# Performance work log

Measured on AMD Instinct MI355X. Metric: run time of the kernel, lower is better.

## Reference

```python
import jax, jax.numpy as jnp
import numpy as np

N = 16384
N_IN = 64
N_H = 64
DIMS = [N_IN, N_H + 200, N_H + 100, N_H]  # 64 -> 264 -> 164 -> 64 (args.l == 2 path)


def setup_inputs() -> dict:
    key = jax.random.key(0)
    ks = jax.random.split(key, 16)
    inp = {
        "seq1": jax.random.normal(ks[0], (1, N, N_IN), dtype=jnp.float32),
        "seq2": jax.random.normal(ks[1], (1, N, N_IN), dtype=jnp.float32),
        # dense adjacency, scaled ~1/n like a row-normalized GCN adjacency
        "adj": jax.random.uniform(ks[2], (1, N, N), dtype=jnp.float32) / N,
        "samp_bias1": jnp.zeros((1, N), dtype=jnp.float32),
        "samp_bias2": jnp.zeros((1, N), dtype=jnp.float32),
    }
    # GCN layer params: Linear(in, out, bias=False) weight + per-layer bias
    for i in range(3):
        din, dout = DIMS[i], DIMS[i + 1]
        inp[f"w{i+1}"] = jax.random.normal(ks[3 + 2 * i], (din, dout), dtype=jnp.float32) * (1.0 / np.sqrt(din))
        inp[f"b{i+1}"] = jnp.zeros((dout,), dtype=jnp.float32)
    # Discriminator bilinear f_k = nn.Bilinear(n_h, n_h, 1): weight [n_h, n_h], bias scalar
    inp["wd"] = jax.random.normal(ks[10], (N_H, N_H), dtype=jnp.float32) * (1.0 / np.sqrt(N_H))
    inp["bd"] = jnp.zeros((), dtype=jnp.float32)
    return inp


def _encoder(seq, adj, ws, bs):
    h = seq  # [1, n, d]
    for w, b in zip(ws, bs):
        # GCN layer: act(adj @ (X W) + b)
        h = jax.nn.relu(jnp.einsum('bnm,bmd->bnd', adj, jnp.einsum('bnk,kd->bnd', h, w)) + b)
    return h


def reference(seq1, seq2, adj, samp_bias1, samp_bias2, w1, b1, w2, b2, w3, b3, wd, bd):
    ws, bs = (w1, w2, w3), (b1, b2, b3)
    h_1 = _encoder(seq1, adj, ws, bs)                 # [1, n, n_h]
    c = jax.nn.sigmoid(jnp.mean(h_1, axis=1))         # AvgReadout + sigmoid -> [1, n_h]
    h_2 = _encoder(seq2, adj, ws, bs)                 # [1, n, n_h]
    # Bilinear discriminator: sc[b, i] = h[b, i, :] @ Wd @ c[b, :] + bd (+ samp_bias)
    cw = jnp.einsum('bd,ed->be', c, wd)               # Wd acts on (h, c) pair -> [1, n_h]
    sc_1 = jnp.einsum('bnd,bd->bn', h_1, cw) + bd + samp_bias1
    sc_2 = jnp.einsum('bnd,bd->bn', h_2, cw) + bd + samp_bias2
    return jnp.concatenate([sc_1, sc_2], axis=1)      # [1, 2n]
```

## Files before the change

### kernel.cpp

```cpp
#include <hip/hip_runtime.h>
#include <hip/hip_bf16.h>

#define NN 16384

using f32x4  = __attribute__((ext_vector_type(4))) float;
using bf16x8 = __attribute__((ext_vector_type(8))) __bf16;
using u16x8  = __attribute__((ext_vector_type(8))) unsigned short;

__device__ __forceinline__ void split2(float x, unsigned short& h, unsigned short& l) {
  unsigned u  = __float_as_uint(x);
  unsigned hu = u & 0xFFFF0000u;
  float lf = x - __uint_as_float(hu);
  __bf16 lb = (__bf16)lf;
  h = (unsigned short)(hu >> 16);
  l = __builtin_bit_cast(unsigned short, lb);
}

__device__ __forceinline__ void gload_lds16(const void* g, void* l) {
  __builtin_amdgcn_global_load_lds(
      (const __attribute__((address_space(1))) unsigned*)g,
      (__attribute__((address_space(3))) unsigned*)l, 16, 0, 0);
}

__global__ void prep_seq(const float* __restrict__ seq1, const float* __restrict__ seq2,
                         unsigned short* __restrict__ Shi, unsigned short* __restrict__ Slo) {
  const int tid = threadIdx.x;
  const int r0  = blockIdx.x * 64;
  const float* seq = blockIdx.y ? seq2 : seq1;
  __shared__ float t[64][65];
  #pragma unroll
  for (int i = 0; i < 16; ++i) {
    int row = i * 4 + (tid >> 6);
    t[row][tid & 63] = seq[(long)(r0 + row) * 64 + (tid & 63)];
  }
  __syncthreads();
  #pragma unroll
  for (int i = 0; i < 16; ++i) {
    int col = i * 4 + (tid >> 6);
    int rr  = tid & 63;
    unsigned short h, l;
    split2(t[rr][col], h, l);
    long o = (long)(blockIdx.y * 64 + col) * NN + r0 + rr;
    Shi[o] = h; Slo[o] = l;
  }
}

__launch_bounds__(256, 2)
__global__ void gemm_adj(const float* __restrict__ A,
                         const unsigned short* __restrict__ Bhi,
                         const unsigned short* __restrict__ Blo,
                         float* __restrict__ P, int ccols, int klen) {
  __shared__ unsigned short Ahs[128 * 40], Als[128 * 40], Xhs[128 * 40], Xls[128 * 40];
  const int tid  = threadIdx.x;
  const int lane = tid & 63;
  const int wave = tid >> 6;
  const int wr = wave & 1;
  const int wc = wave >> 1;
  const int rtile = blockIdx.x * 128;
  const int ctile = blockIdx.y * 128;
  const int kbase = blockIdx.z * klen;

  const int srow  = tid >> 1;
  const int shalf = tid & 1;
  const int wbase = srow * 40 + shalf * 16;

  const float* aptr = A + (long)(rtile + srow) * NN + kbase + shalf * 16;
  const unsigned short* bhp = Bhi + (long)(ctile + srow) * NN + kbase + shalf * 16;
  const unsigned short* blp = Blo + (long)(ctile + srow) * NN + kbase + shalf * 16;

  f32x4 acc[4][4] = {};

  f32x4 a0 = *(const f32x4*)(aptr + 0);
  f32x4 a1 = *(const f32x4*)(aptr + 4);
  f32x4 a2 = *(const f32x4*)(aptr + 8);
  f32x4 a3 = *(const f32x4*)(aptr + 12);
  uint4 bh0 = *(const uint4*)(bhp);
  uint4 bh1 = *(const uint4*)(bhp + 8);
  uint4 bl0 = *(const uint4*)(blp);
  uint4 bl1 = *(const uint4*)(blp + 8);
  aptr += 32; bhp += 32; blp += 32;

  const int nsteps = klen / 32;
  for (int ks = 0; ks < nsteps; ++ks) {
    u16x8 h0, h1, l0, l1;
    #pragma unroll
    for (int i = 0; i < 16; ++i) {
      float x = i < 4 ? a0[i] : (i < 8 ? a1[i - 4] : (i < 12 ? a2[i - 8] : a3[i - 12]));
      unsigned short hh, ll;
      split2(x, hh, ll);
      if (i < 8) { h0[i] = hh; l0[i] = ll; }
      else       { h1[i - 8] = hh; l1[i - 8] = ll; }
    }
    __syncthreads();
    *(u16x8*)&Ahs[wbase + 0] = h0;
    *(u16x8*)&Ahs[wbase + 8] = h1;
    *(u16x8*)&Als[wbase + 0] = l0;
    *(u16x8*)&Als[wbase + 8] = l1;
    *(uint4*)&Xhs[wbase + 0] = bh0;
    *(uint4*)&Xhs[wbase + 8] = bh1;
    *(uint4*)&Xls[wbase + 0] = bl0;
    *(uint4*)&Xls[wbase + 8] = bl1;
    if (ks + 1 < nsteps) {
      a0 = *(const f32x4*)(aptr + 0);
      a1 = *(const f32x4*)(aptr + 4);
      a2 = *(const f32x4*)(aptr + 8);
      a3 = *(const f32x4*)(aptr + 12);
      bh0 = *(const uint4*)(bhp);
      bh1 = *(const uint4*)(bhp + 8);
      bl0 = *(const uint4*)(blp);
      bl1 = *(const uint4*)(blp + 8);
      aptr += 32; bhp += 32; blp += 32;
    }
    __syncthreads();
    bf16x8 ahf[4], alf[4];
    #pragma unroll
    for (int ni = 0; ni < 4; ++ni) {
      int ar  = wr * 64 + ni * 16 + (lane & 15);
      int off = ar * 40 + (lane >> 4) * 8;
      ahf[ni] = *(const bf16x8*)&Ahs[off];
      alf[ni] = *(const bf16x8*)&Als[off];
    }
    #pragma unroll
    for (int mi = 0; mi < 4; ++mi) {
      int xc  = wc * 64 + mi * 16 + (lane & 15);
      int off = xc * 40 + (lane >> 4) * 8;
      bf16x8 xh = *(const bf16x8*)&Xhs[off];
      bf16x8 xl = *(const bf16x8*)&Xls[off];
      #pragma unroll
      for (int ni = 0; ni < 4; ++ni) {
        acc[mi][ni] = __builtin_amdgcn_mfma_f32_16x16x32_bf16(xh, ahf[ni], acc[mi][ni], 0, 0, 0);
        acc[mi][ni] = __builtin_amdgcn_mfma_f32_16x16x32_bf16(xl, ahf[ni], acc[mi][ni], 0, 0, 0);
        acc[mi][ni] = __builtin_amdgcn_mfma_f32_16x16x32_bf16(xh, alf[ni], acc[mi][ni], 0, 0, 0);
      }
    }
  }
  float* out = P + (long)blockIdx.z * ccols * NN;
  #pragma unroll
  for (int mi = 0; mi < 4; ++mi) {
    int xc = ctile + wc * 64 + mi * 16 + ((lane >> 4) << 2);
    #pragma unroll
    for (int ni = 0; ni < 4; ++ni) {
      int ar = rtile + wr * 64 + ni * 16 + (lane & 15);
      #pragma unroll
      for (int j = 0; j < 4; ++j)
        out[(long)(xc + j) * NN + ar] = acc[mi][ni][j];
    }
  }
}

__launch_bounds__(256, 3)
__global__ void gemm_v(const float* __restrict__ A,
                       const unsigned short* __restrict__ Xg,
                       const float* __restrict__ cs,
                       float* __restrict__ P, int ccols, int klen, int nY) {
  __shared__ unsigned short As[128 * 64];
  __shared__ unsigned short Xs[2][128 * 64];
  const int tid  = threadIdx.x;
  const int lane = tid & 63;
  const int wave = tid >> 6;
  const int wr = wave & 1;
  const int wc = wave >> 1;

  int bid = blockIdx.x;
  int lin = (bid & 7) * ((int)gridDim.x >> 3) + (bid >> 3);
  const int by = lin % nY;
  const int bx = (lin / nY) & 127;
  const int bz = lin / (nY * 128);
  const int rtile = bx * 128;
  const int ctile = by * 128;
  const int kbase = bz * klen;

  const int arow0  = wave * 32 + (lane >> 3);
  const int ac     = lane & 7;
  const int awslot = ac ^ (lane >> 3);
  const float* aptr = A + (long)(rtile + arow0) * NN + kbase + ac * 8;

  const int xrow0 = wave * 32 + (lane >> 3);
  const int cx    = (lane & 7) ^ (lane >> 3);
  const unsigned short* xptr = Xg + (long)(ctile + xrow0) * NN + kbase + cx * 8;

  f32x4 acc[4][4] = {};
  f32x4 areg[4][2];

  #pragma unroll
  for (int t = 0; t < 4; ++t) {
    const float* ap = aptr + (long)t * 8 * NN;
    areg[t][0] = *(const f32x4*)ap;
    areg[t][1] = *(const f32x4*)(ap + 4);
    gload_lds16(xptr + (long)t * 8 * NN, &Xs[0][(wave * 4 + t) * 512]);
  }
  aptr += 64; xptr += 64;
  __syncthreads();

  int cur = 0;
  const int nsteps = klen / 64;
  for (int ks = 0; ks < nsteps; ++ks) {
    u16x8 wv[4];
    #pragma unroll
    for (int t = 0; t < 4; ++t) {
      #pragma unroll
      for (int i = 0; i < 8; ++i) {
        float a = (i < 4) ? areg[t][0][i] : areg[t][1][i - 4];
        float v = fmaf(a, 16384.f, -0.5f);
        wv[t][i] = __builtin_bit_cast(unsigned short, (__bf16)v);
      }
    }
    __syncthreads();
    #pragma unroll
    for (int t = 0; t < 4; ++t)
      *(u16x8*)&As[(arow0 + t * 8) * 64 + awslot * 8] = wv[t];
    if (ks + 1 < nsteps) {
      #pragma unroll
      for (int t = 0; t < 4; ++t) {
        gload_lds16(xptr + (long)t * 8 * NN, &Xs[cur ^ 1][(wave * 4 + t) * 512]);
        const float* ap = aptr + (long)t * 8 * NN;
        areg[t][0] = *(const f32x4*)ap;
        areg[t][1] = *(const f32x4*)(ap + 4);
      }
      aptr += 64; xptr += 64;
    }
    __syncthreads();
    #pragma unroll
    for (int mk = 0; mk < 2; ++mk) {
      bf16x8 af[4];
      #pragma unroll
      for (int ni = 0; ni < 4; ++ni) {
        int ar = wr * 64 + ni * 16 + (lane & 15);
        int slot = (mk * 4 + (lane >> 4)) ^ (ar & 7);
        af[ni] = *(const bf16x8*)&As[ar * 64 + slot * 8];
      }
      #pragma unroll
      for (int mi = 0; mi < 4; ++mi) {
        int xr = wc * 64 + mi * 16 + (lane & 15);
        int slot = (mk * 4 + (lane >> 4)) ^ (xr & 7);
        bf16x8 xf = *(const bf16x8*)&Xs[cur][xr * 64 + slot * 8];
        #pragma unroll
        for (int ni = 0; ni < 4; ++ni)
          acc[mi][ni] = __builtin_amdgcn_mfma_f32_16x16x32_bf16(xf, af[ni], acc[mi][ni], 0, 0, 0);
      }
    }
    cur ^= 1;
  }

  const float scl = 1.f / 16384.f;
  float* out = P + (long)bz * ccols * NN;
  #pragma unroll
  for (int mi = 0; mi < 4; ++mi) {
    int xc = ctile + wc * 64 + mi * 16 + ((lane >> 4) << 2);
    float dc[4];
    #pragma unroll
    for (int j = 0; j < 4; ++j) dc[j] = (bz == 0) ? 0.5f * cs[xc + j] : 0.f;
    #pragma unroll
    for (int ni = 0; ni < 4; ++ni) {
      int ar = rtile + wr * 64 + ni * 16 + (lane & 15);
      #pragma unroll
      for (int j = 0; j < 4; ++j)
        out[(long)(xc + j) * NN + ar] = (acc[mi][ni][j] + dc[j]) * scl;
    }
  }
}

__global__ void post1a(const float* __restrict__ P, const float* __restrict__ w1,
                       const float* __restrict__ b1, float* __restrict__ H1T) {
  const int r = blockIdx.x * 256 + threadIdx.x;
  const int e = blockIdx.y;
  for (int c = 0; c < 4; ++c) {
    const int j0 = c * 66;
    float acc[66];
    #pragma unroll
    for (int jj = 0; jj < 66; ++jj) acc[jj] = b1[j0 + jj];
    for (int k = 0; k < 64; ++k) {
      float tv = 0.f;
      #pragma unroll
      for (int z = 0; z < 4; ++z)
        tv += P[(long)(z * 128 + e * 64 + k) * NN + r];
      #pragma unroll
      for (int jj = 0; jj < 66; ++jj)
        acc[jj] = fmaf(tv, w1[k * 264 + j0 + jj], acc[jj]);
    }
    #pragma unroll
    for (int jj = 0; jj < 66; ++jj)
      H1T[(long)(e * 264 + j0 + jj) * NN + r] = fmaxf(acc[jj], 0.f);
  }
}

__global__ void post1b(const float* __restrict__ H1T, const float* __restrict__ w2,
                       unsigned short* __restrict__ G) {
  const int r  = blockIdx.x * 256 + threadIdx.x;
  const int e  = blockIdx.y;
  const int q0 = blockIdx.z * 41;
  float acc[41] = {};
  for (int j = 0; j < 264; ++j) {
    float h = H1T[(long)(e * 264 + j) * NN + r];
    #pragma unroll
    for (int qq = 0; qq < 41; ++qq)
      acc[qq] = fmaf(h, w2[j * 164 + q0 + qq], acc[qq]);
  }
  #pragma unroll
  for (int qq = 0; qq < 41; ++qq)
    G[(long)(e * 192 + q0 + qq) * NN + r] =
        __builtin_bit_cast(unsigned short, (__bf16)acc[qq]);
  if (blockIdx.z == 3) {
    for (int q = 164; q < 192; ++q)
      G[(long)(e * 192 + q) * NN + r] = 0;
  }
}

__global__ void colsum_bf16(const unsigned short* __restrict__ X, float* __restrict__ cs) {
  const int c = blockIdx.x;
  const unsigned short* row = X + (long)c * NN;
  float s = 0.f;
  for (int i = threadIdx.x; i < NN; i += 256)
    s += __uint_as_float((unsigned)row[i] << 16);
  __shared__ float red[256];
  red[threadIdx.x] = s;
  __syncthreads();
  for (int off = 128; off > 0; off >>= 1) {
    if (threadIdx.x < off) red[threadIdx.x] += red[threadIdx.x + off];
    __syncthreads();
  }
  if (threadIdx.x == 0) cs[c] = red[0];
}

__global__ void post2(const float* __restrict__ P, const float* __restrict__ w3,
                      const float* __restrict__ b2, unsigned short* __restrict__ F) {
  const int r = blockIdx.x * 256 + threadIdx.x;
  const int e = blockIdx.y;
  float f[64] = {};
  for (int j = 0; j < 164; ++j) {
    float h = P[(long)(e * 192 + j) * NN + r] + P[(long)(384 + e * 192 + j) * NN + r] + b2[j];
    h = fmaxf(h, 0.f);
    #pragma unroll
    for (int q = 0; q < 64; ++q) f[q] = fmaf(h, w3[j * 64 + q], f[q]);
  }
  #pragma unroll
  for (int q = 0; q < 64; ++q)
    F[(long)(e * 64 + q) * NN + r] = __builtin_bit_cast(unsigned short, (__bf16)f[q]);
}

__global__ void post3(const float* __restrict__ P, const float* __restrict__ b3,
                      float* __restrict__ H3T) {
  const int r = blockIdx.x * 256 + threadIdx.x;
  const int e = blockIdx.y;
  #pragma unroll
  for (int q = 0; q < 64; ++q) {
    float v = b3[q];
    #pragma unroll
    for (int z = 0; z < 4; ++z)
      v += P[(long)(z * 128 + e * 64 + q) * NN + r];
    H3T[(long)(e * 64 + q) * NN + r] = fmaxf(v, 0.f);
  }
}

__global__ void colsum(const float* __restrict__ H3T, float* __restrict__ sums) {
  const int c = blockIdx.x;
  const float* row = H3T + (long)c * NN;
  float s = 0.f;
  for (int i = threadIdx.x; i < NN; i += 256) s += row[i];
  __shared__ float red[256];
  red[threadIdx.x] = s;
  __syncthreads();
  for (int off = 128; off > 0; off >>= 1) {
    if (threadIdx.x < off) red[threadIdx.x] += red[threadIdx.x + off];
    __syncthreads();
  }
  if (threadIdx.x == 0) sums[c] = red[0];
}

__global__ void make_cw(const float* __restrict__ sums, const float* __restrict__ wd,
                        float* __restrict__ cw) {
  __shared__ float cv[64];
  const int t = threadIdx.x;
  cv[t] = 1.f / (1.f + expf(-sums[t] / 16384.f));
  __syncthreads();
  float a = 0.f;
  for (int d = 0; d < 64; ++d) a += cv[d] * wd[t * 64 + d];
  cw[t] = a;
}

__global__ void score(const float* __restrict__ H3T, const float* __restrict__ cw,
                      const float* __restrict__ bdp, const float* __restrict__ sb1,
                      const float* __restrict__ sb2, float* __restrict__ out) {
  const int idx = blockIdx.x * 256 + threadIdx.x;
  const int e = idx >> 14, r = idx & (NN - 1);
  float acc = bdp[0] + (e ? sb2[r] : sb1[r]);
  const float* base = H3T + (long)e * 64 * NN + r;
  #pragma unroll
  for (int j = 0; j < 64; ++j) acc = fmaf(base[(long)j * NN], cw[j], acc);
  out[idx] = acc;
}

extern "C" void kernel_launch(void* const* d_in, const int* in_sizes, int n_in,
                              void* d_out, int out_size, void* d_ws, size_t ws_size,
                              hipStream_t stream) {
  const float* seq1 = (const float*)d_in[0];
  const float* seq2 = (const float*)d_in[1];
  const float* adj  = (const float*)d_in[2];
  const float* sb1  = (const float*)d_in[3];
  const float* sb2  = (const float*)d_in[4];
  const float* w1   = (const float*)d_in[5];
  const float* b1   = (const float*)d_in[6];
  const float* w2   = (const float*)d_in[7];
  const float* b2   = (const float*)d_in[8];
  const float* w3   = (const float*)d_in[9];
  const float* b3   = (const float*)d_in[10];
  const float* wd   = (const float*)d_in[11];
  const float* bd   = (const float*)d_in[12];
  float* out = (float*)d_out;

  char* ws = (char*)d_ws;
  unsigned short* Shi = (unsigned short*)(ws + 0);
  unsigned short* Slo = (unsigned short*)(ws + 4194304);
  float*          Pp  = (float*)(ws + 8388608);
  unsigned short* G   = (unsigned short*)(ws + 58720256);
  float*          H1T = (float*)(ws + 71303168);
  unsigned short* F   = (unsigned short*)(ws + 105906176);
  float*          H3T = (float*)(ws + 110100480);
  float*          csG = (float*)(ws + 118489088);
  float*          csF = (float*)(ws + 118490624);
  float*          sums= (float*)(ws + 118491136);
  float*          cw  = (float*)(ws + 118491392);

  prep_seq   <<<dim3(256, 2), 256, 0, stream>>>(seq1, seq2, Shi, Slo);
  gemm_adj   <<<dim3(128, 1, 4), 256, 0, stream>>>(adj, Shi, Slo, Pp, 128, 4096);
  post1a     <<<dim3(64, 2), 256, 0, stream>>>(Pp, w1, b1, H1T);
  post1b     <<<dim3(64, 2, 4), 256, 0, stream>>>(H1T, w2, G);
  colsum_bf16<<<384, 256, 0, stream>>>(G, csG);
  gemm_v     <<<768, 256, 0, stream>>>(adj, G, csG, Pp, 384, 8192, 3);
  post2      <<<dim3(64, 2), 256, 0, stream>>>(Pp, w3, b2, F);
  colsum_bf16<<<128, 256, 0, stream>>>(F, csF);
  gemm_v     <<<512, 256, 0, stream>>>(adj, F, csF, Pp, 128, 4096, 1);
  post3      <<<dim3(64, 2), 256, 0, stream>>>(Pp, b3, H3T);
  colsum     <<<64, 256, 0, stream>>>(H3T, sums);
  make_cw    <<<1, 64, 0, stream>>>(sums, wd, cw);
  score      <<<128, 256, 0, stream>>>(H3T, cw, bd, sb1, sb2, out);
}
```

Before: 1.250 ms.

## Quantize adjacency to bf16 once in first GEMM and reuse across layers

```diff
diff --git a/kernel.cpp b/kernel.cpp
--- a/kernel.cpp
+++ b/kernel.cpp
@@ -6,15 +6,6 @@
 using f32x4  = __attribute__((ext_vector_type(4))) float;
 using bf16x8 = __attribute__((ext_vector_type(8))) __bf16;
 using u16x8  = __attribute__((ext_vector_type(8))) unsigned short;
-
-__device__ __forceinline__ void split2(float x, unsigned short& h, unsigned short& l) {
-  unsigned u  = __float_as_uint(x);
-  unsigned hu = u & 0xFFFF0000u;
-  float lf = x - __uint_as_float(hu);
-  __bf16 lb = (__bf16)lf;
-  h = (unsigned short)(hu >> 16);
-  l = __builtin_bit_cast(unsigned short, lb);
-}
 
 __device__ __forceinline__ void gload_lds16(const void* g, void* l) {
   __builtin_amdgcn_global_load_lds(
@@ -22,8 +13,42 @@
       (__attribute__((address_space(3))) unsigned*)l, 16, 0, 0);
 }
 
+__device__ __forceinline__ unsigned short bf16r(float x) {
+  return __builtin_bit_cast(unsigned short, (__bf16)x);
+}
+
+__global__ void zero_cs(float* __restrict__ csS) {
+  if (threadIdx.x < 128) csS[threadIdx.x] = 0.f;
+}
+
+__global__ void seqsum(const float* __restrict__ seq1, const float* __restrict__ seq2,
+                       float* __restrict__ csS) {
+  const int e = blockIdx.x >> 4, chunk = blockIdx.x & 15;
+  const float* seq = e ? seq2 : seq1;
+  const int g = threadIdx.x >> 4;
+  const int q = threadIdx.x & 15;
+  f32x4 acc = {};
+  for (int i = 0; i < 64; ++i) {
+    int r = chunk * 1024 + i * 16 + g;
+    acc += *(const f32x4*)(seq + (long)r * 64 + q * 4);
+  }
+  __shared__ f32x4 red[256];
+  red[threadIdx.x] = acc;
+  __syncthreads();
+  if (threadIdx.x < 64) {
+    int d = threadIdx.x;
+    float s = 0.f;
+    #pragma unroll
+    for (int g2 = 0; g2 < 16; ++g2) {
+      f32x4 v = red[g2 * 16 + (d >> 2)];
+      s += v[d & 3];
+    }
+    atomicAdd(&csS[e * 64 + d], s);
+  }
+}
+
 __global__ void prep_seq(const float* __restrict__ seq1, const float* __restrict__ seq2,
-                         unsigned short* __restrict__ Shi, unsigned short* __restrict__ Slo) {
+                         unsigned short* __restrict__ Shi) {
   const int tid = threadIdx.x;
   const int r0  = blockIdx.x * 64;
   const float* seq = blockIdx.y ? seq2 : seq1;
@@ -38,118 +63,124 @@
   for (int i = 0; i < 16; ++i) {
     int col = i * 4 + (tid >> 6);
     int rr  = tid & 63;
-    unsigned short h, l;
-    split2(t[rr][col], h, l);
-    long o = (long)(blockIdx.y * 64 + col) * NN + r0 + rr;
-    Shi[o] = h; Slo[o] = l;
-  }
-}
-
-__launch_bounds__(256, 2)
-__global__ void gemm_adj(const float* __restrict__ A,
-                         const unsigned short* __restrict__ Bhi,
-                         const unsigned short* __restrict__ Blo,
-                         float* __restrict__ P, int ccols, int klen) {
-  __shared__ unsigned short Ahs[128 * 40], Als[128 * 40], Xhs[128 * 40], Xls[128 * 40];
+    Shi[(long)(blockIdx.y * 64 + col) * NN + r0 + rr] = bf16r(t[rr][col]);
+  }
+}
+
+__launch_bounds__(256, 3)
+__global__ void gemm1(const float* __restrict__ A,
+                      const unsigned short* __restrict__ Xg,
+                      const float* __restrict__ cs,
+                      float* __restrict__ P,
+                      unsigned short* __restrict__ Vg) {
+  __shared__ unsigned short As[128 * 64];
+  __shared__ unsigned short Xs[2][128 * 64];
   const int tid  = threadIdx.x;
   const int lane = tid & 63;
   const int wave = tid >> 6;
   const int wr = wave & 1;
   const int wc = wave >> 1;
-  const int rtile = blockIdx.x * 128;
-  const int ctile = blockIdx.y * 128;
-  const int kbase = blockIdx.z * klen;
-
-  const int srow  = tid >> 1;
-  const int shalf = tid & 1;
-  const int wbase = srow * 40 + shalf * 16;
-
-  const float* aptr = A + (long)(rtile + srow) * NN + kbase + shalf * 16;
-  const unsigned short* bhp = Bhi + (long)(ctile + srow) * NN + kbase + shalf * 16;
-  const unsigned short* blp = Blo + (long)(ctile + srow) * NN + kbase + shalf * 16;
+
+  int bid = blockIdx.x;
+  int lin = (bid & 7) * ((int)gridDim.x >> 3) + (bid >> 3);
+  const int bx = lin & 127;
+  const int bz = lin >> 7;
+  const int rtile = bx * 128;
+  const int kbase = bz * 4096;
+
+  const int arow0  = wave * 32 + (lane >> 3);
+  const int ac     = lane & 7;
+  const int awslot = ac ^ (lane >> 3);
+  const float* aptr = A + (long)(rtile + arow0) * NN + kbase + ac * 8;
+  unsigned short* vptr = Vg + (long)(rtile + arow0) * NN + kbase + ac * 8;
+
+  const int cx = (lane & 7) ^ (lane >> 3);
+  const unsigned short* xptr = Xg + (long)arow0 * NN + kbase + cx * 8;
 
   f32x4 acc[4][4] = {};
-
-  f32x4 a0 = *(const f32x4*)(aptr + 0);
-  f32x4 a1 = *(const f32x4*)(aptr + 4);
-  f32x4 a2 = *(const f32x4*)(aptr + 8);
-  f32x4 a3 = *(const f32x4*)(aptr + 12);
-  uint4 bh0 = *(const uint4*)(bhp);
-  uint4 bh1 = *(const uint4*)(bhp + 8);
-  uint4 bl0 = *(const uint4*)(blp);
-  uint4 bl1 = *(const uint4*)(blp + 8);
-  aptr += 32; bhp += 32; blp += 32;
-
-  const int nsteps = klen / 32;
+  f32x4 areg[4][2];
+
+  #pragma unroll
+  for (int t = 0; t < 4; ++t) {
+    const float* ap = aptr + (long)t * 8 * NN;
+    areg[t][0] = *(const f32x4*)ap;
+    areg[t][1] = *(const f32x4*)(ap + 4);
+    gload_lds16(xptr + (long)t * 8 * NN, &Xs[0][(wave * 4 + t) * 512]);
+  }
+  aptr += 64; xptr += 64;
+  __syncthreads();
+
+  int cur = 0;
+  const int nsteps = 4096 / 64;
   for (int ks = 0; ks < nsteps; ++ks) {
-    u16x8 h0, h1, l0, l1;
-    #pragma unroll
-    for (int i = 0; i < 16; ++i) {
-      float x = i < 4 ? a0[i] : (i < 8 ? a1[i - 4] : (i < 12 ? a2[i - 8] : a3[i - 12]));
-      unsigned short hh, ll;
-      split2(x, hh, ll);
-      if (i < 8) { h0[i] = hh; l0[i] = ll; }
-      else       { h1[i - 8] = hh; l1[i - 8] = ll; }
-    }
-    __syncthreads();
-    *(u16x8*)&Ahs[wbase + 0] = h0;
-    *(u16x8*)&Ahs[wbase + 8] = h1;
-    *(u16x8*)&Als[wbase + 0] = l0;
-    *(u16x8*)&Als[wbase + 8] = l1;
-    *(uint4*)&Xhs[wbase + 0] = bh0;
-    *(uint4*)&Xhs[wbase + 8] = bh1;
-    *(uint4*)&Xls[wbase + 0] = bl0;
-    *(uint4*)&Xls[wbase + 8] = bl1;
+    u16x8 wv[4];
+    #pragma unroll
+    for (int t = 0; t < 4; ++t) {
+      #pragma unroll
+      for (int i = 0; i < 8; ++i) {
+        float a = (i < 4) ? areg[t][0][i] : areg[t][1][i - 4];
+        wv[t][i] = bf16r(fmaf(a, 16384.f, -0.5f));
+      }
+      *(u16x8*)(vptr + (long)t * 8 * NN) = wv[t];
+    }
+    vptr += 64;
+    __syncthreads();
+    #pragma unroll
+    for (int t = 0; t < 4; ++t)
+      *(u16x8*)&As[(arow0 + t * 8) * 64 + awslot * 8] = wv[t];
     if (ks + 1 < nsteps) {
-      a0 = *(const f32x4*)(aptr + 0);
-      a1 = *(const f32x4*)(aptr + 4);
-      a2 = *(const f32x4*)(aptr + 8);
-      a3 = *(const f32x4*)(aptr + 12);
-      bh0 = *(const uint4*)(bhp);
-      bh1 = *(const uint4*)(bhp + 8);
-      bl0 = *(const uint4*)(blp);
-      bl1 = *(const uint4*)(blp + 8);
-      aptr += 32; bhp += 32; blp += 32;
-    }
-    __syncthreads();
-    bf16x8 ahf[4], alf[4];
-    #pragma unroll
-    for (int ni = 0; ni < 4; ++ni) {
-      int ar  = wr * 64 + ni * 16 + (lane & 15);
-      int off = ar * 40 + (lane >> 4) * 8;
-      ahf[ni] = *(const bf16x8*)&Ahs[off];
-      alf[ni] = *(const bf16x8*)&Als[off];
-    }
-    #pragma unroll
-    for (int mi = 0; mi < 4; ++mi) {
-      int xc  = wc * 64 + mi * 16 + (lane & 15);
-      int off = xc * 40 + (lane >> 4) * 8;
-      bf16x8 xh = *(const bf16x8*)&Xhs[off];
-      bf16x8 xl = *(const bf16x8*)&Xls[off];
+      #pragma unroll
+      for (int t = 0; t < 4; ++t) {
+        gload_lds16(xptr + (long)t * 8 * NN, &Xs[cur ^ 1][(wave * 4 + t) * 512]);
+        const float* ap = aptr + (long)t * 8 * NN;
+        areg[t][0] = *(const f32x4*)ap;
+        areg[t][1] = *(const f32x4*)(ap + 4);
+      }
+      aptr += 64; xptr += 64;
+    }
+    __syncthreads();
+    #pragma unroll
+    for (int mk = 0; mk < 2; ++mk) {
+      bf16x8 af[4];
       #pragma unroll
       for (int ni = 0; ni < 4; ++ni) {
-        acc[mi][ni] = __builtin_amdgcn_mfma_f32_16x16x32_bf16(xh, ahf[ni], acc[mi][ni], 0, 0, 0);
-        acc[mi][ni] = __builtin_amdgcn_mfma_f32_16x16x32_bf16(xl, ahf[ni], acc[mi][ni], 0, 0, 0);
-        acc[mi][ni] = __builtin_amdgcn_mfma_f32_16x16x32_bf16(xh, alf[ni], acc[mi][ni], 0, 0, 0);
-      }
-    }
-  }
-  float* out = P + (long)blockIdx.z * ccols * NN;
+        int ar = wr * 64 + ni * 16 + (lane & 15);
+        int slot = (mk * 4 + (lane >> 4)) ^ (ar & 7);
+        af[ni] = *(const bf16x8*)&As[ar * 64 + slot * 8];
+      }
+      #pragma unroll
+      for (int mi = 0; mi < 4; ++mi) {
+        int xr = wc * 64 + mi * 16 + (lane & 15);
+        int slot = (mk * 4 + (lane >> 4)) ^ (xr & 7);
+        bf16x8 xf = *(const bf16x8*)&Xs[cur][xr * 64 + slot * 8];
+        #pragma unroll
+        for (int ni = 0; ni < 4; ++ni)
+          acc[mi][ni] = __builtin_amdgcn_mfma_f32_16x16x32_bf16(xf, af[ni], acc[mi][ni], 0, 0, 0);
+      }
+    }
+    cur ^= 1;
+  }
+
+  const float scl = 1.f / 16384.f;
+  float* out = P + (long)bz * 128 * NN;
   #pragma unroll
   for (int mi = 0; mi < 4; ++mi) {
-    int xc = ctile + wc * 64 + mi * 16 + ((lane >> 4) << 2);
+    int xc = wc * 64 + mi * 16 + ((lane >> 4) << 2);
+    float dc[4];
+    #pragma unroll
+    for (int j = 0; j < 4; ++j) dc[j] = (bz == 0) ? 0.5f * cs[xc + j] : 0.f;
     #pragma unroll
     for (int ni = 0; ni < 4; ++ni) {
       int ar = rtile + wr * 64 + ni * 16 + (lane & 15);
       #pragma unroll
       for (int j = 0; j < 4; ++j)
-        out[(long)(xc + j) * NN + ar] = acc[mi][ni][j];
+        out[(long)(xc + j) * NN + ar] = (acc[mi][ni][j] + dc[j]) * scl;
     }
   }
 }
 
 __launch_bounds__(256, 3)
-__global__ void gemm_v(const float* __restrict__ A,
+__global__ void gemm23(const unsigned short* __restrict__ Va,
                        const unsigned short* __restrict__ Xg,
                        const float* __restrict__ cs,
                        float* __restrict__ P, int ccols, int klen, int nY) {
@@ -173,20 +204,17 @@
   const int arow0  = wave * 32 + (lane >> 3);
   const int ac     = lane & 7;
   const int awslot = ac ^ (lane >> 3);
-  const float* aptr = A + (long)(rtile + arow0) * NN + kbase + ac * 8;
-
-  const int xrow0 = wave * 32 + (lane >> 3);
-  const int cx    = (lane & 7) ^ (lane >> 3);
-  const unsigned short* xptr = Xg + (long)(ctile + xrow0) * NN + kbase + cx * 8;
+  const unsigned short* aptr = Va + (long)(rtile + arow0) * NN + kbase + ac * 8;
+
+  const int cx = (lane & 7) ^ (lane >> 3);
+  const unsigned short* xptr = Xg + (long)(ctile + arow0) * NN + kbase + cx * 8;
 
   f32x4 acc[4][4] = {};
-  f32x4 areg[4][2];
+  u16x8 av[4];
 
   #pragma unroll
   for (int t = 0; t < 4; ++t) {
-    const float* ap = aptr + (long)t * 8 * NN;
-    areg[t][0] = *(const f32x4*)ap;
-    areg[t][1] = *(const f32x4*)(ap + 4);
+    av[t] = *(const u16x8*)(aptr + (long)t * 8 * NN);
     gload_lds16(xptr + (long)t * 8 * NN, &Xs[0][(wave * 4 + t) * 512]);
   }
   aptr += 64; xptr += 64;
@@ -195,27 +223,15 @@
   int cur = 0;
   const int nsteps = klen / 64;
   for (int ks = 0; ks < nsteps; ++ks) {
-    u16x8 wv[4];
-    #pragma unroll
-    for (int t = 0; t < 4; ++t) {
-      #pragma unroll
-      for (int i = 0; i < 8; ++i) {
-        float a = (i < 4) ? areg[t][0][i] : areg[t][1][i - 4];
-        float v = fmaf(a, 16384.f, -0.5f);
-        wv[t][i] = __builtin_bit_cast(unsigned short, (__bf16)v);
-      }
-    }
     __syncthreads();
     #pragma unroll
     for (int t = 0; t < 4; ++t)
-      *(u16x8*)&As[(arow0 + t * 8) * 64 + awslot * 8] = wv[t];
+      *(u16x8*)&As[(arow0 + t * 8) * 64 + awslot * 8] = av[t];
     if (ks + 1 < nsteps) {
       #pragma unroll
       for (int t = 0; t < 4; ++t) {
         gload_lds16(xptr + (long)t * 8 * NN, &Xs[cur ^ 1][(wave * 4 + t) * 512]);
-        const float* ap = aptr + (long)t * 8 * NN;
-        areg[t][0] = *(const f32x4*)ap;
-        areg[t][1] = *(const f32x4*)(ap + 4);
+        av[t] = *(const u16x8*)(aptr + (long)t * 8 * NN);
       }
       aptr += 64; xptr += 64;
     }
@@ -264,7 +280,7 @@
                        const float* __restrict__ b1, float* __restrict__ H1T) {
   const int r = blockIdx.x * 256 + threadIdx.x;
   const int e = blockIdx.y;
-  for (int c = 0; c < 4; ++c) {
+  for (int c = blockIdx.z * 2; c < blockIdx.z * 2 + 2; ++c) {
     const int j0 = c * 66;
     float acc[66];
     #pragma unroll
@@ -298,8 +314,7 @@
   }
   #pragma unroll
   for (int qq = 0; qq < 41; ++qq)
-    G[(long)(e * 192 + q0 + qq) * NN + r] =
-        __builtin_bit_cast(unsigned short, (__bf16)acc[qq]);
+    G[(long)(e * 192 + q0 + qq) * NN + r] = bf16r(acc[qq]);
   if (blockIdx.z == 3) {
     for (int q = 164; q < 192; ++q)
       G[(long)(e * 192 + q) * NN + r] = 0;
@@ -324,18 +339,19 @@
 
 __global__ void post2(const float* __restrict__ P, const float* __restrict__ w3,
                       const float* __restrict__ b2, unsigned short* __restrict__ F) {
-  const int r = blockIdx.x * 256 + threadIdx.x;
-  const int e = blockIdx.y;
-  float f[64] = {};
+  const int r  = blockIdx.x * 256 + threadIdx.x;
+  const int e  = blockIdx.y;
+  const int q0 = blockIdx.z * 32;
+  float f[32] = {};
   for (int j = 0; j < 164; ++j) {
     float h = P[(long)(e * 192 + j) * NN + r] + P[(long)(384 + e * 192 + j) * NN + r] + b2[j];
     h = fmaxf(h, 0.f);
     #pragma unroll
-    for (int q = 0; q < 64; ++q) f[q] = fmaf(h, w3[j * 64 + q], f[q]);
-  }
-  #pragma unroll
-  for (int q = 0; q < 64; ++q)
-    F[(long)(e * 64 + q) * NN + r] = __builtin_bit_cast(unsigned short, (__bf16)f[q]);
+    for (int q = 0; q < 32; ++q) f[q] = fmaf(h, w3[j * 64 + q0 + q], f[q]);
+  }
+  #pragma unroll
+  for (int q = 0; q < 32; ++q)
+    F[(long)(e * 64 + q0 + q) * NN + r] = bf16r(f[q]);
 }
 
 __global__ void post3(const float* __restrict__ P, const float* __restrict__ b3,
@@ -409,27 +425,30 @@
   float* out = (float*)d_out;
 
   char* ws = (char*)d_ws;
-  unsigned short* Shi = (unsigned short*)(ws + 0);
-  unsigned short* Slo = (unsigned short*)(ws + 4194304);
-  float*          Pp  = (float*)(ws + 8388608);
-  unsigned short* G   = (unsigned short*)(ws + 58720256);
-  float*          H1T = (float*)(ws + 71303168);
-  unsigned short* F   = (unsigned short*)(ws + 105906176);
-  float*          H3T = (float*)(ws + 110100480);
-  float*          csG = (float*)(ws + 118489088);
-  float*          csF = (float*)(ws + 118490624);
-  float*          sums= (float*)(ws + 118491136);
-  float*          cw  = (float*)(ws + 118491392);
-
-  prep_seq   <<<dim3(256, 2), 256, 0, stream>>>(seq1, seq2, Shi, Slo);
-  gemm_adj   <<<dim3(128, 1, 4), 256, 0, stream>>>(adj, Shi, Slo, Pp, 128, 4096);
-  post1a     <<<dim3(64, 2), 256, 0, stream>>>(Pp, w1, b1, H1T);
+  unsigned short* Vg  = (unsigned short*)(ws + 0);
+  unsigned short* Shi = (unsigned short*)(ws + 536870912);
+  float*          Pp  = (float*)(ws + 541065216);
+  unsigned short* G   = (unsigned short*)(ws + 591396864);
+  float*          H1T = (float*)(ws + 603979776);
+  unsigned short* F   = (unsigned short*)(ws + 638582784);
+  float*          H3T = (float*)(ws + 642777088);
+  float*          csS = (float*)(ws + 651165696);
+  float*          csG = (float*)(ws + 651166208);
+  float*          csF = (float*)(ws + 651167744);
+  float*          sums= (float*)(ws + 651168256);
+  float*          cw  = (float*)(ws + 651168512);
+
+  zero_cs    <<<1, 128, 0, stream>>>(csS);
+  seqsum     <<<32, 256, 0, stream>>>(seq1, seq2, csS);
+  prep_seq   <<<dim3(256, 2), 256, 0, stream>>>(seq1, seq2, Shi);
+  gemm1      <<<512, 256, 0, stream>>>(adj, Shi, csS, Pp, Vg);
+  post1a     <<<dim3(64, 2, 2), 256, 0, stream>>>(Pp, w1, b1, H1T);
   post1b     <<<dim3(64, 2, 4), 256, 0, stream>>>(H1T, w2, G);
   colsum_bf16<<<384, 256, 0, stream>>>(G, csG);
-  gemm_v     <<<768, 256, 0, stream>>>(adj, G, csG, Pp, 384, 8192, 3);
-  post2      <<<dim3(64, 2), 256, 0, stream>>>(Pp, w3, b2, F);
+  gemm23     <<<768, 256, 0, stream>>>(Vg, G, csG, Pp, 384, 8192, 3);
+  post2      <<<dim3(64, 2, 2), 256, 0, stream>>>(Pp, w3, b2, F);
   colsum_bf16<<<128, 256, 0, stream>>>(F, csF);
-  gemm_v     <<<512, 256, 0, stream>>>(adj, F, csF, Pp, 128, 4096, 1);
+  gemm23     <<<512, 256, 0, stream>>>(Vg, F, csF, Pp, 128, 4096, 1);
   post3      <<<dim3(64, 2), 256, 0, stream>>>(Pp, b3, H3T);
   colsum     <<<64, 256, 0, stream>>>(H3T, sums);
   make_cw    <<<1, 64, 0, stream>>>(sums, wd, cw);
```

Measured after the change: 1.116 ms. 10.7% less time.
